# Kernel tuning notes

Hardware: AMD Instinct MI355X
Metric: run time of the kernel (lower is better)

## Reference

```python
import jax, jax.numpy as jnp
import numpy as np

N_NODES = 100000


def gcn_conv(x, W, b, src, dst, n_nodes):
    """PyG GCNConv: add self-loops, symmetric normalization, linear, scatter-add, bias."""
    xw = x @ W  # [N, out]
    loop = jnp.arange(n_nodes, dtype=src.dtype)
    src2 = jnp.concatenate([src, loop])  # sources (x_j gathered from here)
    dst2 = jnp.concatenate([dst, loop])  # targets (aggregation index)
    # degree (incl. self-loops) computed at target nodes, unit edge weights
    deg = jax.ops.segment_sum(jnp.ones_like(dst2, dtype=xw.dtype), dst2, num_segments=n_nodes)
    dinv = jnp.where(deg > 0, jax.lax.rsqrt(deg), 0.0)
    norm = dinv[src2] * dinv[dst2]  # [E+N]
    msg = xw[src2] * norm[:, None]  # [E+N, out]  (memory-bound gather)
    out = jax.ops.segment_sum(msg, dst2, num_segments=n_nodes)  # scatter-add
    return out + b


def setup_inputs() -> dict:
    key = jax.random.key(0)
    k1, k2, k3, k4 = jax.random.split(key, 4)
    F_IN, H, C = 128, 128, 64
    E = 1600000
    x = jax.random.normal(k1, (N_NODES, F_IN), dtype=jnp.float32)
    edge_index = jax.random.randint(k2, (2, E), 0, N_NODES, dtype=jnp.int64)
    # Glorot init like PyG GCNConv
    s1 = float(np.sqrt(6.0 / (F_IN + H)))
    s2 = float(np.sqrt(6.0 / (H + C)))
    W1 = jax.random.uniform(k3, (F_IN, H), jnp.float32, -s1, s1)
    W2 = jax.random.uniform(k4, (H, C), jnp.float32, -s2, s2)
    b1 = jnp.zeros((H,), jnp.float32)
    b2 = jnp.zeros((C,), jnp.float32)
    return {"x": x, "edge_index": edge_index, "W1": W1, "b1": b1, "W2": W2, "b2": b2}


def reference(x, edge_index, W1, b1, W2, b2):
    src, dst = edge_index[0], edge_index[1]
    h = gcn_conv(x, W1, b1, src, dst, N_NODES)
    h = jax.nn.relu(h)  # dropout p=0.0 -> identity
    h = gcn_conv(h, W2, b2, src, dst, N_NODES)
    return jax.nn.log_softmax(h, axis=1)
```

## Files before the change

### kernel.cpp

```cpp
#include <hip/hip_runtime.h>
#include <cmath>


#define THREADS 256
#define BSHIFT 8
#define MAXB 512
#define PADSLACK 1792

__device__ __forceinline__ unsigned short f2bf(float f) {
    union { float f; unsigned u; } v; v.f = f;
    unsigned r = v.u + 0x7FFFu + ((v.u >> 16) & 1u);
    return (unsigned short)(r >> 16);
}
__device__ __forceinline__ float bf_lo(unsigned u) {
    union { unsigned u; float f; } v; v.u = u << 16; return v.f;
}
__device__ __forceinline__ float bf_hi(unsigned u) {
    union { unsigned u; float f; } v; v.u = u & 0xFFFF0000u; return v.f;
}

__global__ __launch_bounds__(256) void k_bcount(const int* __restrict__ dst, int E, int B,
                                                int* __restrict__ bcnt) {
    __shared__ int lc[MAXB];
    for (int i = threadIdx.x; i < MAXB; i += 256) lc[i] = 0;
    __syncthreads();
    for (int e = blockIdx.x * blockDim.x + threadIdx.x; e < E; e += gridDim.x * blockDim.x)
        atomicAdd(&lc[dst[e] >> BSHIFT], 1);
    __syncthreads();
    for (int b = threadIdx.x; b < B; b += 256)
        if (lc[b]) atomicAdd(&bcnt[b], lc[b]);
}

__global__ void k_bscan(const int* __restrict__ bcnt, int B, int* __restrict__ boff) {
    __shared__ int sh[MAXB];
    const int t = threadIdx.x;
    int v = (t < B) ? bcnt[t] : 0;
    sh[t] = v; __syncthreads();
    for (int o = 1; o < MAXB; o <<= 1) {
        int add = (t >= o) ? sh[t - o] : 0;
        __syncthreads();
        sh[t] += add;
        __syncthreads();
    }
    if (t < B) boff[t] = sh[t] - v;
    if (t == B - 1) boff[B] = sh[t];
}

__global__ __launch_bounds__(256) void k_bscatter(const int* __restrict__ src,
                                                  const int* __restrict__ dst, int E, int B,
                                                  const int* __restrict__ boff,
                                                  int* __restrict__ bfill,
                                                  unsigned* __restrict__ pairs) {
    __shared__ int lc[MAXB];
    __shared__ int lbase[MAXB];
    const int tid = threadIdx.x;
    const int e0 = blockIdx.x * 8192;
    for (int i = tid; i < MAXB; i += 256) lc[i] = 0;
    __syncthreads();
#pragma unroll
    for (int k = 0; k < 32; k++) {
        int e = e0 + k * 256 + tid;
        if (e < E) atomicAdd(&lc[dst[e] >> BSHIFT], 1);
    }
    __syncthreads();
    for (int b = tid; b < B; b += 256)
        lbase[b] = lc[b] ? atomicAdd(&bfill[b], lc[b]) : 0;
    __syncthreads();
    for (int i = tid; i < MAXB; i += 256) lc[i] = 0;
    __syncthreads();
#pragma unroll
    for (int k = 0; k < 32; k++) {
        int e = e0 + k * 256 + tid;
        if (e < E) {
            int s = src[e], d = dst[e];
            int b = d >> BSHIFT;
            int r = atomicAdd(&lc[b], 1);
            pairs[(size_t)boff[b] + lbase[b] + r] =
                ((unsigned)(d & 255) << 24) | (unsigned)s;
        }
    }
}

__global__ __launch_bounds__(256) void k_bbuild(const unsigned* __restrict__ pairs,
                                                const int* __restrict__ boff, int N,
                                                int* __restrict__ deg,
                                                float* __restrict__ dinv,
                                                int* __restrict__ rowptr,
                                                unsigned* __restrict__ csr_off) {
    __shared__ int ldeg[256], lex[256], lrank[256];
    const int b = blockIdx.x, tid = threadIdx.x;
    const int node0 = b << BSHIFT;
    const int base = boff[b];
    const int pbase = base + b * PADSLACK;
    const int cnt_e = boff[b + 1] - base;
    ldeg[tid] = 0;
    __syncthreads();
    for (int e = tid; e < cnt_e; e += 256)
        atomicAdd(&ldeg[pairs[base + e] >> 24], 1);
    __syncthreads();
    int v = ldeg[tid];
    int pd = (v + 7) & ~7;
    lex[tid] = pd; __syncthreads();
    for (int o = 1; o < 256; o <<= 1) {
        int add = (tid >= o) ? lex[tid - o] : 0;
        __syncthreads();
        lex[tid] += add;
        __syncthreads();
    }
    int pexcl = lex[tid] - pd;
    if (node0 + tid < N) {
        deg[node0 + tid] = v;
        dinv[node0 + tid] = rsqrtf((float)(v + 1));
        rowptr[node0 + tid] = pbase + pexcl;
    }
    __syncthreads();
    lex[tid] = pexcl;
    lrank[tid] = 0;
    __syncthreads();
    for (int e = tid; e < cnt_e; e += 256) {
        unsigned p = pairs[base + e];
        int loc = p >> 24;
        int r = atomicAdd(&lrank[loc], 1);
        csr_off[pbase + lex[loc] + r] = (p & 0xFFFFFFu) << 8;
    }
    for (int p = v; p < pd; p++)
        csr_off[pbase + pexcl + p] = ((unsigned)N) << 8;
}

__global__ void k_castW(const float* __restrict__ W1, const float* __restrict__ W2,
                        unsigned short* __restrict__ Wt1, unsigned short* __restrict__ Wt2) {
    int idx = blockIdx.x * blockDim.x + threadIdx.x;
    if (idx < 16384) {
        int n = idx >> 7, k = idx & 127;
        Wt1[idx] = f2bf(W1[k * 128 + n]);
    } else if (idx < 16384 + 8192) {
        int t = idx - 16384;
        int n = t >> 7, k = t & 127;
        Wt2[t] = f2bf(W2[k * 64 + n]);
    }
}

typedef __attribute__((ext_vector_type(8))) short bf16x8;
typedef __attribute__((ext_vector_type(4))) float f32x4;

template <int NC, bool A_BF16>
__global__ __launch_bounds__(256) void k_gemm_mfma(const void* __restrict__ Av,
                                                   const unsigned short* __restrict__ Wt,
                                                   const float* __restrict__ dinv,
                                                   unsigned short* __restrict__ Out,
                                                   unsigned short* __restrict__ zrow,
                                                   int M) {
    constexpr int KP = 136;
    __shared__ __align__(16) short Bs[NC * KP];
    const int tid = threadIdx.x;
    const int row0 = blockIdx.x * 64;

    if (blockIdx.x == 0 && tid < NC) zrow[tid] = 0;

    for (int f = tid; f < NC * 16; f += 256) {
        int n = f >> 4, c = (f & 15) * 8;
        *(uint4*)&Bs[n * KP + c] = *(const uint4*)&Wt[n * 128 + c];
    }

    const int wave = tid >> 6, lane = tid & 63;
    const int m = lane & 15, quad = lane >> 4;
    const int row = row0 + 16 * wave + m;
    const int rowc = row < M ? row : (M - 1);

    bf16x8 afr[4];
    if (A_BF16) {
        const unsigned short* A = (const unsigned short*)Av;
#pragma unroll
        for (int k = 0; k < 4; k++)
            afr[k] = *(const bf16x8*)&A[(size_t)rowc * 128 + quad * 8 + 32 * k];
    } else {
        const float* A = (const float*)Av;
#pragma unroll
        for (int k = 0; k < 4; k++) {
            float4 lo = *(const float4*)&A[(size_t)rowc * 128 + quad * 8 + 32 * k];
            float4 hi = *(const float4*)&A[(size_t)rowc * 128 + quad * 8 + 32 * k + 4];
            bf16x8 a;
            a[0] = (short)f2bf(lo.x); a[1] = (short)f2bf(lo.y);
            a[2] = (short)f2bf(lo.z); a[3] = (short)f2bf(lo.w);
            a[4] = (short)f2bf(hi.x); a[5] = (short)f2bf(hi.y);
            a[6] = (short)f2bf(hi.z); a[7] = (short)f2bf(hi.w);
            afr[k] = a;
        }
    }
    __syncthreads();

    constexpr int CT = NC / 16;
    f32x4 acc[CT] = {};
    const short* brow = &Bs[m * KP + quad * 8];
#pragma unroll
    for (int k = 0; k < 4; k++) {
#pragma unroll
        for (int c = 0; c < CT; c++) {
            bf16x8 b = *(const bf16x8*)&brow[(size_t)c * 16 * KP + 32 * k];
            acc[c] = __builtin_amdgcn_mfma_f32_16x16x32_bf16(afr[k], b, acc[c], 0, 0, 0);
        }
    }

    __syncthreads();
    short* Cs = Bs;
    const int rbase = 16 * wave + quad * 4;
    float dv[4];
#pragma unroll
    for (int r = 0; r < 4; r++) {
        int gr = row0 + rbase + r;
        dv[r] = dinv[gr < M ? gr : 0];
    }
#pragma unroll
    for (int c = 0; c < CT; c++)
#pragma unroll
        for (int r = 0; r < 4; r++)
            Cs[(rbase + r) * NC + 16 * c + m] = (short)f2bf(acc[c][r] * dv[r]);
    __syncthreads();
    for (int f = tid; f < 64 * NC / 8; f += 256) {
        int r = f / (NC / 8), c = (f % (NC / 8)) * 8;
        if (row0 + r < M)
            *(uint4*)&Out[(size_t)(row0 + r) * NC + c] = *(const uint4*)&Cs[r * NC + c];
    }
}

__global__ __launch_bounds__(256) void k_agg128b(const unsigned* __restrict__ csr_off,
                                                 const int* __restrict__ rowptr,
                                                 const int* __restrict__ cnt,
                                                 const float* __restrict__ dinv,
                                                 const unsigned char* __restrict__ xwb,
                                                 const float* __restrict__ bias,
                                                 unsigned* __restrict__ h1, int N) {
    const int lane = threadIdx.x & 63;
    const int wid = (blockIdx.x * blockDim.x + threadIdx.x) >> 6;
    const int g = lane >> 4, sl = lane & 15;
    const int i = wid * 4 + g;
    if (i >= N) return;
    const float di = dinv[i];
    const int slb = sl * 16;
    uint4 u = *(const uint4*)(xwb + ((size_t)i << 8) + slb);
    float a0 = bf_lo(u.x), a1 = bf_hi(u.x), a2 = bf_lo(u.y), a3 = bf_hi(u.y);
    float a4 = bf_lo(u.z), a5 = bf_hi(u.z), a6 = bf_lo(u.w), a7 = bf_hi(u.w);
    const int start = rowptr[i];
    const int pc = (cnt[i] + 7) & ~7;
    unsigned s[8];
#pragma unroll
    for (int k = 0; k < 8; k++) s[k] = csr_off[start + k];
    for (int j = 0; j < pc; j += 8) {
        uint4 uu[8];
#pragma unroll
        for (int k = 0; k < 8; k++) uu[k] = *(const uint4*)(xwb + s[k] + slb);
#pragma unroll
        for (int k = 0; k < 8; k++) s[k] = csr_off[start + j + 8 + k];
#pragma unroll
        for (int k = 0; k < 8; k++) {
            a0 += bf_lo(uu[k].x); a1 += bf_hi(uu[k].x);
            a2 += bf_lo(uu[k].y); a3 += bf_hi(uu[k].y);
            a4 += bf_lo(uu[k].z); a5 += bf_hi(uu[k].z);
            a6 += bf_lo(uu[k].w); a7 += bf_hi(uu[k].w);
        }
    }
    float4 b0 = *(const float4*)&bias[8 * sl];
    float4 b1 = *(const float4*)&bias[8 * sl + 4];
    float r0 = fmaxf(di * a0 + b0.x, 0.f);
    float r1 = fmaxf(di * a1 + b0.y, 0.f);
    float r2 = fmaxf(di * a2 + b0.z, 0.f);
    float r3 = fmaxf(di * a3 + b0.w, 0.f);
    float r4 = fmaxf(di * a4 + b1.x, 0.f);
    float r5 = fmaxf(di * a5 + b1.y, 0.f);
    float r6 = fmaxf(di * a6 + b1.z, 0.f);
    float r7 = fmaxf(di * a7 + b1.w, 0.f);
    uint4 o;
    o.x = (unsigned)f2bf(r0) | ((unsigned)f2bf(r1) << 16);
    o.y = (unsigned)f2bf(r2) | ((unsigned)f2bf(r3) << 16);
    o.z = (unsigned)f2bf(r4) | ((unsigned)f2bf(r5) << 16);
    o.w = (unsigned)f2bf(r6) | ((unsigned)f2bf(r7) << 16);
    *(uint4*)&h1[(size_t)i * 64 + 4 * sl] = o;
}

__global__ __launch_bounds__(256) void k_agg64b(const unsigned* __restrict__ csr_off,
                                                const int* __restrict__ rowptr,
                                                const int* __restrict__ cnt,
                                                const float* __restrict__ dinv,
                                                const unsigned char* __restrict__ xwb,
                                                const float* __restrict__ bias,
                                                float* __restrict__ out, int N) {
    const int lane = threadIdx.x & 63;
    const int wid = (blockIdx.x * blockDim.x + threadIdx.x) >> 6;
    const int g = lane >> 3, sl = lane & 7;
    const int i = wid * 8 + g;
    if (i >= N) return;
    const float di = dinv[i];
    const int slb = sl * 16;
    uint4 u = *(const uint4*)(xwb + ((size_t)i << 7) + slb);
    float a0 = bf_lo(u.x), a1 = bf_hi(u.x), a2 = bf_lo(u.y), a3 = bf_hi(u.y);
    float a4 = bf_lo(u.z), a5 = bf_hi(u.z), a6 = bf_lo(u.w), a7 = bf_hi(u.w);
    const int start = rowptr[i];
    const int pc = (cnt[i] + 7) & ~7;
    unsigned s[8];
#pragma unroll
    for (int k = 0; k < 8; k++) s[k] = csr_off[start + k];
    for (int j = 0; j < pc; j += 8) {
        uint4 uu[8];
#pragma unroll
        for (int k = 0; k < 8; k++) uu[k] = *(const uint4*)(xwb + (s[k] >> 1) + slb);
#pragma unroll
        for (int k = 0; k < 8; k++) s[k] = csr_off[start + j + 8 + k];
#pragma unroll
        for (int k = 0; k < 8; k++) {
            a0 += bf_lo(uu[k].x); a1 += bf_hi(uu[k].x);
            a2 += bf_lo(uu[k].y); a3 += bf_hi(uu[k].y);
            a4 += bf_lo(uu[k].z); a5 += bf_hi(uu[k].z);
            a6 += bf_lo(uu[k].w); a7 += bf_hi(uu[k].w);
        }
    }
    float4 b0 = *(const float4*)&bias[8 * sl];
    float4 b1 = *(const float4*)&bias[8 * sl + 4];
    float v0 = di * a0 + b0.x, v1 = di * a1 + b0.y;
    float v2 = di * a2 + b0.z, v3 = di * a3 + b0.w;
    float v4 = di * a4 + b1.x, v5 = di * a5 + b1.y;
    float v6 = di * a6 + b1.z, v7 = di * a7 + b1.w;
    float m = fmaxf(fmaxf(fmaxf(v0, v1), fmaxf(v2, v3)),
                    fmaxf(fmaxf(v4, v5), fmaxf(v6, v7)));
#pragma unroll
    for (int o = 4; o > 0; o >>= 1) m = fmaxf(m, __shfl_xor(m, o));
    float s2 = expf(v0 - m) + expf(v1 - m) + expf(v2 - m) + expf(v3 - m) +
               expf(v4 - m) + expf(v5 - m) + expf(v6 - m) + expf(v7 - m);
#pragma unroll
    for (int o = 4; o > 0; o >>= 1) s2 += __shfl_xor(s2, o);
    float ls = m + logf(s2);
    *(float4*)&out[(size_t)i * 64 + 8 * sl] = make_float4(v0 - ls, v1 - ls, v2 - ls, v3 - ls);
    *(float4*)&out[(size_t)i * 64 + 8 * sl + 4] = make_float4(v4 - ls, v5 - ls, v6 - ls, v7 - ls);
}

extern "C" void kernel_launch(void* const* d_in, const int* in_sizes, int n_in,
                              void* d_out, int out_size, void* d_ws, size_t ws_size,
                              hipStream_t stream) {
    const float* x  = (const float*)d_in[0];
    const int*   ei = (const int*)d_in[1];
    const float* W1 = (const float*)d_in[2];
    const float* b1 = (const float*)d_in[3];
    const float* W2 = (const float*)d_in[4];
    const float* b2 = (const float*)d_in[5];

    const int N = in_sizes[0] / 128;
    const int E = in_sizes[1] / 2;
    const int* src = ei;
    const int* dst = ei + E;
    const int B = (N + 255) >> BSHIFT;

    char* ws = (char*)d_ws;
    size_t off = 0;
    auto alloc = [&](size_t bytes) {
        void* p = ws + off;
        off += (bytes + 255) & ~(size_t)255;
        return p;
    };
    int*            bcnt    = (int*)alloc(MAXB * 4 * 2);
    int*            bfill   = bcnt + MAXB;
    int*            boff    = (int*)alloc((MAXB + 1) * 4);
    int*            deg     = (int*)alloc((size_t)N * 4);
    float*          dinv    = (float*)alloc((size_t)N * 4);
    int*            rowptr  = (int*)alloc((size_t)N * 4);
    unsigned*       csr_off = (unsigned*)alloc(((size_t)E + (size_t)B * PADSLACK + 64) * 4);
    unsigned*       pairs   = (unsigned*)alloc((size_t)E * 4);
    unsigned short* Wt1     = (unsigned short*)alloc(128 * 128 * 2);
    unsigned short* Wt2     = (unsigned short*)alloc(64 * 128 * 2);
    unsigned short* xw1     = (unsigned short*)alloc((size_t)(N + 1) * 128 * 2);
    unsigned short* h1      = (unsigned short*)alloc((size_t)N * 128 * 2);
    unsigned short* hw2     = xw1;
    float*          out     = (float*)d_out;

    hipMemsetAsync(bcnt, 0, MAXB * 4 * 2, stream);

    k_bcount<<<512, THREADS, 0, stream>>>(dst, E, B, bcnt);
    k_bscan<<<1, MAXB, 0, stream>>>(bcnt, B, boff);
    k_bscatter<<<(E + 8191) / 8192, THREADS, 0, stream>>>(src, dst, E, B, boff, bfill, pairs);
    k_bbuild<<<B, THREADS, 0, stream>>>(pairs, boff, N, deg, dinv, rowptr, csr_off);

    k_castW<<<96, THREADS, 0, stream>>>(W1, W2, Wt1, Wt2);

    const int agg128Blocks = (N + 15) / 16;
    const int agg64Blocks  = (N + 31) / 32;

    k_gemm_mfma<128, false><<<(N + 63) / 64, THREADS, 0, stream>>>(
        x, Wt1, dinv, xw1, xw1 + (size_t)N * 128, N);
    k_agg128b<<<agg128Blocks, THREADS, 0, stream>>>(
        csr_off, rowptr, deg, dinv, (const unsigned char*)xw1, b1, (unsigned*)h1, N);

    k_gemm_mfma<64, true><<<(N + 63) / 64, THREADS, 0, stream>>>(
        h1, Wt2, dinv, hw2, hw2 + (size_t)N * 64, N);
    k_agg64b<<<agg64Blocks, THREADS, 0, stream>>>(
        csr_off, rowptr, deg, dinv, (const unsigned char*)hw2, b2, out, N);
}
```

Before: 275.0 us.

## Fuse CSR preprocessing kernels using fixed-size bucket slabs and global degree atomics

```diff
diff --git a/kernel.cpp b/kernel.cpp
--- a/kernel.cpp
+++ b/kernel.cpp
@@ -5,7 +5,9 @@
 #define THREADS 256
 #define BSHIFT 8
 #define MAXB 512
-#define PADSLACK 1792
+#define SLAB_E 8192
+#define SLAB_C 9984
+#define NB_CAST 96
 
 __device__ __forceinline__ unsigned short f2bf(float f) {
     union { float f; unsigned u; } v; v.f = f;
@@ -19,48 +21,42 @@
     union { unsigned u; float f; } v; v.u = u & 0xFFFF0000u; return v.f;
 }
 
-__global__ __launch_bounds__(256) void k_bcount(const int* __restrict__ dst, int E, int B,
-                                                int* __restrict__ bcnt) {
-    __shared__ int lc[MAXB];
-    for (int i = threadIdx.x; i < MAXB; i += 256) lc[i] = 0;
-    __syncthreads();
-    for (int e = blockIdx.x * blockDim.x + threadIdx.x; e < E; e += gridDim.x * blockDim.x)
-        atomicAdd(&lc[dst[e] >> BSHIFT], 1);
-    __syncthreads();
-    for (int b = threadIdx.x; b < B; b += 256)
-        if (lc[b]) atomicAdd(&bcnt[b], lc[b]);
-}
-
-__global__ void k_bscan(const int* __restrict__ bcnt, int B, int* __restrict__ boff) {
-    __shared__ int sh[MAXB];
-    const int t = threadIdx.x;
-    int v = (t < B) ? bcnt[t] : 0;
-    sh[t] = v; __syncthreads();
-    for (int o = 1; o < MAXB; o <<= 1) {
-        int add = (t >= o) ? sh[t - o] : 0;
-        __syncthreads();
-        sh[t] += add;
-        __syncthreads();
-    }
-    if (t < B) boff[t] = sh[t] - v;
-    if (t == B - 1) boff[B] = sh[t];
-}
-
-__global__ __launch_bounds__(256) void k_bscatter(const int* __restrict__ src,
-                                                  const int* __restrict__ dst, int E, int B,
-                                                  const int* __restrict__ boff,
-                                                  int* __restrict__ bfill,
-                                                  unsigned* __restrict__ pairs) {
-    __shared__ int lc[MAXB];
-    __shared__ int lbase[MAXB];
+__global__ __launch_bounds__(256) void k_prep(const int* __restrict__ src,
+                                              const int* __restrict__ dst, int E, int B,
+                                              const float* __restrict__ W1,
+                                              const float* __restrict__ W2,
+                                              unsigned short* __restrict__ Wt1,
+                                              unsigned short* __restrict__ Wt2,
+                                              int* __restrict__ bfill,
+                                              int* __restrict__ deg,
+                                              unsigned* __restrict__ pairs) {
+    __shared__ int lc[MAXB], lbase[MAXB];
     const int tid = threadIdx.x;
-    const int e0 = blockIdx.x * 8192;
+    if (blockIdx.x < NB_CAST) {
+        int idx = blockIdx.x * 256 + tid;
+        if (idx < 16384) {
+            int n = idx >> 7, k = idx & 127;
+            Wt1[idx] = f2bf(W1[k * 128 + n]);
+        } else {
+            int t = idx - 16384;
+            int n = t >> 7, k = t & 127;
+            Wt2[t] = f2bf(W2[k * 64 + n]);
+        }
+        return;
+    }
+    const int e0 = (blockIdx.x - NB_CAST) * 8192;
     for (int i = tid; i < MAXB; i += 256) lc[i] = 0;
     __syncthreads();
 #pragma unroll
-    for (int k = 0; k < 32; k++) {
-        int e = e0 + k * 256 + tid;
-        if (e < E) atomicAdd(&lc[dst[e] >> BSHIFT], 1);
+    for (int k = 0; k < 8; k++) {
+        int e = e0 + k * 1024 + tid * 4;
+        if (e < E) {
+            int4 d4 = *(const int4*)&dst[e];
+            atomicAdd(&lc[d4.x >> BSHIFT], 1); atomicAdd(&lc[d4.y >> BSHIFT], 1);
+            atomicAdd(&lc[d4.z >> BSHIFT], 1); atomicAdd(&lc[d4.w >> BSHIFT], 1);
+            atomicAdd(&deg[d4.x], 1); atomicAdd(&deg[d4.y], 1);
+            atomicAdd(&deg[d4.z], 1); atomicAdd(&deg[d4.w], 1);
+        }
     }
     __syncthreads();
     for (int b = tid; b < B; b += 256)
@@ -69,34 +65,38 @@
     for (int i = tid; i < MAXB; i += 256) lc[i] = 0;
     __syncthreads();
 #pragma unroll
-    for (int k = 0; k < 32; k++) {
-        int e = e0 + k * 256 + tid;
+    for (int k = 0; k < 8; k++) {
+        int e = e0 + k * 1024 + tid * 4;
         if (e < E) {
-            int s = src[e], d = dst[e];
-            int b = d >> BSHIFT;
-            int r = atomicAdd(&lc[b], 1);
-            pairs[(size_t)boff[b] + lbase[b] + r] =
-                ((unsigned)(d & 255) << 24) | (unsigned)s;
-        }
-    }
-}
-
-__global__ __launch_bounds__(256) void k_bbuild(const unsigned* __restrict__ pairs,
-                                                const int* __restrict__ boff, int N,
-                                                int* __restrict__ deg,
-                                                float* __restrict__ dinv,
-                                                int* __restrict__ rowptr,
-                                                unsigned* __restrict__ csr_off) {
-    __shared__ int ldeg[256], lex[256], lrank[256];
+            int4 s4 = *(const int4*)&src[e];
+            int4 d4 = *(const int4*)&dst[e];
+            int b0, r;
+            b0 = d4.x >> BSHIFT; r = atomicAdd(&lc[b0], 1);
+            pairs[(size_t)b0 * SLAB_E + lbase[b0] + r] = ((unsigned)(d4.x & 255) << 24) | (unsigned)s4.x;
+            b0 = d4.y >> BSHIFT; r = atomicAdd(&lc[b0], 1);
+            pairs[(size_t)b0 * SLAB_E + lbase[b0] + r] = ((unsigned)(d4.y & 255) << 24) | (unsigned)s4.y;
+            b0 = d4.z >> BSHIFT; r = atomicAdd(&lc[b0], 1);
+            pairs[(size_t)b0 * SLAB_E + lbase[b0] + r] = ((unsigned)(d4.z & 255) << 24) | (unsigned)s4.z;
+            b0 = d4.w >> BSHIFT; r = atomicAdd(&lc[b0], 1);
+            pairs[(size_t)b0 * SLAB_E + lbase[b0] + r] = ((unsigned)(d4.w & 255) << 24) | (unsigned)s4.w;
+        }
+    }
+}
+
+__device__ __forceinline__ void bbuild_body(int* sm, const unsigned* __restrict__ pairs,
+                                            const int* __restrict__ bfill, int N,
+                                            int* __restrict__ rowptr,
+                                            unsigned* __restrict__ csr_off) {
+    int* ldeg = sm; int* lex = sm + 256; int* lrank = sm + 512;
     const int b = blockIdx.x, tid = threadIdx.x;
     const int node0 = b << BSHIFT;
-    const int base = boff[b];
-    const int pbase = base + b * PADSLACK;
-    const int cnt_e = boff[b + 1] - base;
+    const unsigned* pb = pairs + (size_t)b * SLAB_E;
+    const int cnt_e = bfill[b];
+    const int pbase = b * SLAB_C;
     ldeg[tid] = 0;
     __syncthreads();
     for (int e = tid; e < cnt_e; e += 256)
-        atomicAdd(&ldeg[pairs[base + e] >> 24], 1);
+        atomicAdd(&ldeg[pb[e] >> 24], 1);
     __syncthreads();
     int v = ldeg[tid];
     int pd = (v + 7) & ~7;
@@ -108,54 +108,36 @@
         __syncthreads();
     }
     int pexcl = lex[tid] - pd;
-    if (node0 + tid < N) {
-        deg[node0 + tid] = v;
-        dinv[node0 + tid] = rsqrtf((float)(v + 1));
-        rowptr[node0 + tid] = pbase + pexcl;
-    }
+    if (node0 + tid < N) rowptr[node0 + tid] = pbase + pexcl;
     __syncthreads();
     lex[tid] = pexcl;
     lrank[tid] = 0;
     __syncthreads();
     for (int e = tid; e < cnt_e; e += 256) {
-        unsigned p = pairs[base + e];
+        unsigned p = pb[e];
         int loc = p >> 24;
         int r = atomicAdd(&lrank[loc], 1);
         csr_off[pbase + lex[loc] + r] = (p & 0xFFFFFFu) << 8;
     }
-    for (int p = v; p < pd; p++)
-        csr_off[pbase + pexcl + p] = ((unsigned)N) << 8;
-}
-
-__global__ void k_castW(const float* __restrict__ W1, const float* __restrict__ W2,
-                        unsigned short* __restrict__ Wt1, unsigned short* __restrict__ Wt2) {
-    int idx = blockIdx.x * blockDim.x + threadIdx.x;
-    if (idx < 16384) {
-        int n = idx >> 7, k = idx & 127;
-        Wt1[idx] = f2bf(W1[k * 128 + n]);
-    } else if (idx < 16384 + 8192) {
-        int t = idx - 16384;
-        int n = t >> 7, k = t & 127;
-        Wt2[t] = f2bf(W2[k * 64 + n]);
-    }
+    for (int p2 = v; p2 < pd; p2++)
+        csr_off[pbase + pexcl + p2] = ((unsigned)N) << 8;
 }
 
 typedef __attribute__((ext_vector_type(8))) short bf16x8;
 typedef __attribute__((ext_vector_type(4))) float f32x4;
 
 template <int NC, bool A_BF16>
-__global__ __launch_bounds__(256) void k_gemm_mfma(const void* __restrict__ Av,
-                                                   const unsigned short* __restrict__ Wt,
-                                                   const float* __restrict__ dinv,
-                                                   unsigned short* __restrict__ Out,
-                                                   unsigned short* __restrict__ zrow,
-                                                   int M) {
+__device__ __forceinline__ void gemm_body(char* smem, int bid, const void* __restrict__ Av,
+                                          const unsigned short* __restrict__ Wt,
+                                          const int* __restrict__ deg,
+                                          unsigned short* __restrict__ Out,
+                                          unsigned short* __restrict__ zrow, int M) {
     constexpr int KP = 136;
-    __shared__ __align__(16) short Bs[NC * KP];
+    short* Bs = (short*)smem;
     const int tid = threadIdx.x;
-    const int row0 = blockIdx.x * 64;
-
-    if (blockIdx.x == 0 && tid < NC) zrow[tid] = 0;
+    const int row0 = bid * 64;
+
+    if (bid == 0 && tid < NC) zrow[tid] = 0;
 
     for (int f = tid; f < NC * 16; f += 256) {
         int n = f >> 4, c = (f & 15) * 8;
@@ -208,7 +190,7 @@
 #pragma unroll
     for (int r = 0; r < 4; r++) {
         int gr = row0 + rbase + r;
-        dv[r] = dinv[gr < M ? gr : 0];
+        dv[r] = rsqrtf((float)(deg[gr < M ? gr : 0] + 1));
     }
 #pragma unroll
     for (int c = 0; c < CT; c++)
@@ -223,10 +205,34 @@
     }
 }
 
+__global__ __launch_bounds__(256) void k_build_gemm1(const unsigned* __restrict__ pairs,
+                                                     const int* __restrict__ bfill, int B, int N,
+                                                     int* __restrict__ rowptr,
+                                                     unsigned* __restrict__ csr_off,
+                                                     const float* __restrict__ x,
+                                                     const unsigned short* __restrict__ Wt1,
+                                                     const int* __restrict__ deg,
+                                                     unsigned short* __restrict__ xw1,
+                                                     unsigned short* __restrict__ zrow) {
+    __shared__ __align__(16) char smem[128 * 136 * 2];
+    if ((int)blockIdx.x < B)
+        bbuild_body((int*)smem, pairs, bfill, N, rowptr, csr_off);
+    else
+        gemm_body<128, false>(smem, blockIdx.x - B, x, Wt1, deg, xw1, zrow, N);
+}
+
+__global__ __launch_bounds__(256) void k_gemm2(const unsigned short* __restrict__ h1,
+                                               const unsigned short* __restrict__ Wt2,
+                                               const int* __restrict__ deg,
+                                               unsigned short* __restrict__ hw2,
+                                               unsigned short* __restrict__ zrow, int M) {
+    __shared__ __align__(16) char smem[64 * 136 * 2];
+    gemm_body<64, true>(smem, blockIdx.x, h1, Wt2, deg, hw2, zrow, M);
+}
+
 __global__ __launch_bounds__(256) void k_agg128b(const unsigned* __restrict__ csr_off,
                                                  const int* __restrict__ rowptr,
-                                                 const int* __restrict__ cnt,
-                                                 const float* __restrict__ dinv,
+                                                 const int* __restrict__ deg,
                                                  const unsigned char* __restrict__ xwb,
                                                  const float* __restrict__ bias,
                                                  unsigned* __restrict__ h1, int N) {
@@ -235,13 +241,14 @@
     const int g = lane >> 4, sl = lane & 15;
     const int i = wid * 4 + g;
     if (i >= N) return;
-    const float di = dinv[i];
+    const int dgi = deg[i];
+    const float di = rsqrtf((float)(dgi + 1));
     const int slb = sl * 16;
     uint4 u = *(const uint4*)(xwb + ((size_t)i << 8) + slb);
     float a0 = bf_lo(u.x), a1 = bf_hi(u.x), a2 = bf_lo(u.y), a3 = bf_hi(u.y);
     float a4 = bf_lo(u.z), a5 = bf_hi(u.z), a6 = bf_lo(u.w), a7 = bf_hi(u.w);
     const int start = rowptr[i];
-    const int pc = (cnt[i] + 7) & ~7;
+    const int pc = (dgi + 7) & ~7;
     unsigned s[8];
 #pragma unroll
     for (int k = 0; k < 8; k++) s[k] = csr_off[start + k];
@@ -279,8 +286,7 @@
 
 __global__ __launch_bounds__(256) void k_agg64b(const unsigned* __restrict__ csr_off,
                                                 const int* __restrict__ rowptr,
-                                                const int* __restrict__ cnt,
-                                                const float* __restrict__ dinv,
+                                                const int* __restrict__ deg,
                                                 const unsigned char* __restrict__ xwb,
                                                 const float* __restrict__ bias,
                                                 float* __restrict__ out, int N) {
@@ -289,13 +295,14 @@
     const int g = lane >> 3, sl = lane & 7;
     const int i = wid * 8 + g;
     if (i >= N) return;
-    const float di = dinv[i];
+    const int dgi = deg[i];
+    const float di = rsqrtf((float)(dgi + 1));
     const int slb = sl * 16;
     uint4 u = *(const uint4*)(xwb + ((size_t)i << 7) + slb);
     float a0 = bf_lo(u.x), a1 = bf_hi(u.x), a2 = bf_lo(u.y), a3 = bf_hi(u.y);
     float a4 = bf_lo(u.z), a5 = bf_hi(u.z), a6 = bf_lo(u.w), a7 = bf_hi(u.w);
     const int start = rowptr[i];
-    const int pc = (cnt[i] + 7) & ~7;
+    const int pc = (dgi + 7) & ~7;
     unsigned s[8];
 #pragma unroll
     for (int k = 0; k < 8; k++) s[k] = csr_off[start + k];
@@ -355,40 +362,31 @@
         off += (bytes + 255) & ~(size_t)255;
         return p;
     };
-    int*            bcnt    = (int*)alloc(MAXB * 4 * 2);
-    int*            bfill   = bcnt + MAXB;
-    int*            boff    = (int*)alloc((MAXB + 1) * 4);
-    int*            deg     = (int*)alloc((size_t)N * 4);
-    float*          dinv    = (float*)alloc((size_t)N * 4);
+    int*            bfill   = (int*)alloc((MAXB + (size_t)N) * 4);
+    int*            deg     = bfill + MAXB;
     int*            rowptr  = (int*)alloc((size_t)N * 4);
-    unsigned*       csr_off = (unsigned*)alloc(((size_t)E + (size_t)B * PADSLACK + 64) * 4);
-    unsigned*       pairs   = (unsigned*)alloc((size_t)E * 4);
+    unsigned*       csr_off = (unsigned*)alloc(((size_t)B * SLAB_C + 64) * 4);
+    unsigned*       pairs   = (unsigned*)alloc((size_t)B * SLAB_E * 4);
     unsigned short* Wt1     = (unsigned short*)alloc(128 * 128 * 2);
     unsigned short* Wt2     = (unsigned short*)alloc(64 * 128 * 2);
     unsigned short* xw1     = (unsigned short*)alloc((size_t)(N + 1) * 128 * 2);
     unsigned short* h1      = (unsigned short*)alloc((size_t)N * 128 * 2);
     unsigned short* hw2     = xw1;
-    float*          out     = (float*)d_out;
-
-    hipMemsetAsync(bcnt, 0, MAXB * 4 * 2, stream);
-
-    k_bcount<<<512, THREADS, 0, stream>>>(dst, E, B, bcnt);
-    k_bscan<<<1, MAXB, 0, stream>>>(bcnt, B, boff);
-    k_bscatter<<<(E + 8191) / 8192, THREADS, 0, stream>>>(src, dst, E, B, boff, bfill, pairs);
-    k_bbuild<<<B, THREADS, 0, stream>>>(pairs, boff, N, deg, dinv, rowptr, csr_off);
-
-    k_castW<<<96, THREADS, 0, stream>>>(W1, W2, Wt1, Wt2);
-
-    const int agg128Blocks = (N + 15) / 16;
-    const int agg64Blocks  = (N + 31) / 32;
-
-    k_gemm_mfma<128, false><<<(N + 63) / 64, THREADS, 0, stream>>>(
-        x, Wt1, dinv, xw1, xw1 + (size_t)N * 128, N);
-    k_agg128b<<<agg128Blocks, THREADS, 0, stream>>>(
-        csr_off, rowptr, deg, dinv, (const unsigned char*)xw1, b1, (unsigned*)h1, N);
-
-    k_gemm_mfma<64, true><<<(N + 63) / 64, THREADS, 0, stream>>>(
-        h1, Wt2, dinv, hw2, hw2 + (size_t)N * 64, N);
-    k_agg64b<<<agg64Blocks, THREADS, 0, stream>>>(
-        csr_off, rowptr, deg, dinv, (const unsigned char*)hw2, b2, out, N);
-}
+    float*          outp    = (float*)d_out;
+
+    hipMemsetAsync(bfill, 0, (MAXB + (size_t)N) * 4, stream);
+
+    const int NB_SCAT = (E + 8191) / 8192;
+    const int NB_GEMM = (N + 63) / 64;
+
+    k_prep<<<NB_CAST + NB_SCAT, THREADS, 0, stream>>>(src, dst, E, B, W1, W2, Wt1, Wt2,
+                                                      bfill, deg, pairs);
+    k_build_gemm1<<<B + NB_GEMM, THREADS, 0, stream>>>(pairs, bfill, B, N, rowptr, csr_off,
+                                                       x, Wt1, deg, xw1,
+                                                       xw1 + (size_t)N * 128);
+    k_agg128b<<<(N + 15) / 16, THREADS, 0, stream>>>(
+        csr_off, rowptr, deg, (const unsigned char*)xw1, b1, (unsigned*)h1, N);
+    k_gemm2<<<NB_GEMM, THREADS, 0, stream>>>(h1, Wt2, deg, hw2, hw2 + (size_t)N * 64, N);
+    k_agg64b<<<(N + 31) / 32, THREADS, 0, stream>>>(
+        csr_off, rowptr, deg, (const unsigned char*)hw2, b2, outp, N);
+}
```

New measurement: 302.4 us. 1.1x slower.
